# Kernel tuning notes

Measured on AMD Instinct MI355X. Metric: run time of the kernel, lower is better.

## Reference

```python
import jax, jax.numpy as jnp
import numpy as np

# S5 layer: ZOH discretization of diagonal complex SSM + parallel associative scan
# u: (B, L, H) real; state dim P (complex diagonal Lambda)

DT_MIN, DT_MAX = 1e-3, 1e-1
STEP_RESCALE = 1.0

def setup_inputs() -> dict:
    key = jax.random.key(0)
    ks = jax.random.split(key, 7)
    Bsz, L, H, P = 8, 4096, 1024, 512
    u = jax.random.normal(ks[0], (Bsz, L, H), jnp.float32)
    # HiPPO-like diagonal: negative real part, spread imaginary part
    Lambda_re = -0.5 * jnp.abs(jax.random.normal(ks[1], (P,), jnp.float32)) - 0.1
    Lambda_im = jnp.pi * jax.random.normal(ks[2], (P,), jnp.float32)
    # B: (P, H, 2) real/imag stacked (xavier-ish scale); C: (H, P, 2)
    Bp = jax.random.normal(ks[3], (P, H, 2), jnp.float32) / np.sqrt(H)
    Cp = jax.random.normal(ks[4], (H, P, 2), jnp.float32) / np.sqrt(P)
    D = jax.random.normal(ks[5], (H,), jnp.float32)
    log_step = jnp.log(jax.random.uniform(ks[6], (P, 1), jnp.float32) * (DT_MAX - DT_MIN) + DT_MIN)
    return {"u": u, "Lambda_re": Lambda_re, "Lambda_im": Lambda_im,
            "B": Bp, "C": Cp, "D": D, "log_step": log_step}


def _s5_forward(u, Lambda_re, Lambda_im, B, C, D, log_step):
    # clip_eigs=True: keep real part strictly negative
    Lambda = jnp.minimum(Lambda_re, -1e-4) + 1j * Lambda_im          # (P,)
    B_tilde = (B[..., 0] + 1j * B[..., 1]).astype(jnp.complex64)      # (P, H)
    C_tilde = (C[..., 0] + 1j * C[..., 1]).astype(jnp.complex64)      # (H, P)
    step = STEP_RESCALE * jnp.exp(log_step[:, 0])                     # (P,)
    # ZOH discretization
    Lambda_bar = jnp.exp(Lambda * step)                               # (P,)
    B_bar = ((Lambda_bar - 1.0) / Lambda)[:, None] * B_tilde          # (P, H)
    # input projection into state space
    Bu = jnp.einsum('blh,ph->blp', u.astype(jnp.complex64), B_bar)    # (B, L, P)
    A = jnp.broadcast_to(Lambda_bar, Bu.shape)                        # (B, L, P)
    # linear recurrence x_k = Lambda_bar * x_{k-1} + Bu_k via log-depth scan
    def combine(e_i, e_j):
        a_i, b_i = e_i
        a_j, b_j = e_j
        return a_j * a_i, a_j * b_i + b_j
    _, xs = jax.lax.associative_scan(combine, (A, Bu), axis=1)        # (B, L, P)
    # readout
    ys = jnp.einsum('blp,hp->blh', xs, C_tilde).real + D * u          # (B, L, H)
    return ys


def reference(u, Lambda_re, Lambda_im, B, C, D, log_step):
    return _s5_forward(u, Lambda_re, Lambda_im, B, C, D, log_step)
```

## Files before the change

### kernel.cpp

```cpp
#include <hip/hip_runtime.h>


#define Bsz 8
#define Lseq 4096
#define Hdim 1024
#define Pdim 512
#define NCHUNK 64
#define CHUNK 64
#define MROWS 32768

typedef __attribute__((ext_vector_type(8))) __bf16 bf16x8;
typedef __attribute__((ext_vector_type(4))) float f32x4;

__device__ __forceinline__ unsigned short f2bf(float f) {
  union { float f; unsigned u; } v; v.f = f;
  unsigned r = v.u + 0x7fffu + ((v.u >> 16) & 1u);
  return (unsigned short)(r >> 16);
}
__device__ __forceinline__ float bf2f(unsigned short s) {
  union { unsigned u; float f; } v; v.u = ((unsigned)s) << 16;
  return v.f;
}

__device__ __forceinline__ void gld_lds16(const void* g, void* l) {
  __builtin_amdgcn_global_load_lds(
      (const __attribute__((address_space(1))) unsigned int*)g,
      (__attribute__((address_space(3))) unsigned int*)l, 16, 0, 0);
}

__global__ void k_setup(const float* __restrict__ Lre_in, const float* __restrict__ Lim_in,
                        const float* __restrict__ log_step,
                        float2* __restrict__ a_arr, float2* __restrict__ aS_arr,
                        float2* __restrict__ g_arr) {
  int p = threadIdx.x;
  if (p >= Pdim) return;
  float lre = fminf(Lre_in[p], -1e-4f);
  float lim = Lim_in[p];
  float step = expf(log_step[p]);
  float zr = lre * step, zi = lim * step;
  float er = expf(zr);
  float ar = er * cosf(zi), ai = er * sinf(zi);
  a_arr[p] = make_float2(ar, ai);
  float erS = expf(zr * (float)CHUNK);
  aS_arr[p] = make_float2(erS * cosf(zi * (float)CHUNK), erS * sinf(zi * (float)CHUNK));
  float den = lre * lre + lim * lim;
  float nr = ar - 1.0f, ni = ai;
  g_arr[p] = make_float2((nr * lre + ni * lim) / den, (ni * lre - nr * lim) / den);
}

__global__ void k_prep_B(const float* __restrict__ Bin, const float2* __restrict__ g_arr,
                         unsigned short* __restrict__ Bbar2) {
  int idx = blockIdx.x * 256 + threadIdx.x;
  int p = idx >> 10;
  int h = idx & 1023;
  float B0 = Bin[2 * idx];
  float B1 = Bin[2 * idx + 1];
  float2 g = g_arr[p];
  Bbar2[(size_t)p * Hdim + h]            = f2bf(g.x * B0 - g.y * B1);
  Bbar2[(size_t)(Pdim + p) * Hdim + h]   = f2bf(g.x * B1 + g.y * B0);
}

__global__ void k_prep_C(const float* __restrict__ Cin, unsigned short* __restrict__ C2m) {
  int idx = blockIdx.x * 256 + threadIdx.x;
  int h = idx >> 9;
  int p = idx & 511;
  float C0 = Cin[2 * idx];
  float C1 = Cin[2 * idx + 1];
  C2m[(size_t)h * 1024 + p]        = f2bf(C0);
  C2m[(size_t)h * 1024 + 512 + p]  = f2bf(-C1);
}

__global__ void k_cvt_u(const float* __restrict__ u, unsigned short* __restrict__ ub) {
  size_t i = ((size_t)blockIdx.x * 256 + threadIdx.x) * 4;
  float4 v = *(const float4*)(u + i);
  ushort4 o;
  o.x = f2bf(v.x); o.y = f2bf(v.y); o.z = f2bf(v.z); o.w = f2bf(v.w);
  *(ushort4*)(ub + i) = o;
}

template <int EPI>
__global__ __launch_bounds__(256, 5) void gemm_bt(const unsigned short* __restrict__ A,
                                                  const unsigned short* __restrict__ Bt,
                                                  void* __restrict__ Cout,
                                                  const float* __restrict__ uin,
                                                  const float* __restrict__ Dvec) {
  const int K = 1024;
  __shared__ __align__(16) unsigned short sm[16384];
  char* smc = (char*)sm;

  int tid = threadIdx.x;
  int lane = tid & 63;
  int w = tid >> 6;
  int wr = w >> 1, wc = w & 1;
  int quad = lane >> 4;
  int mrow = lane & 15;

  int wg = blockIdx.x;
  size_t rowBase = (size_t)(wg >> 3) * 128;
  size_t colBase = (size_t)(wg & 7) * 128;

  f32x4 acc[4][4];
#pragma unroll
  for (int i = 0; i < 4; i++)
#pragma unroll
    for (int j = 0; j < 4; j++) acc[i][j] = (f32x4){0.f, 0.f, 0.f, 0.f};

  int r0 = tid >> 2;
  int cst = (tid & 3) ^ ((tid >> 3) & 3);
  const unsigned short* pa0 = A + rowBase * K + (size_t)r0 * K + cst * 8;
  const unsigned short* pa1 = pa0 + (size_t)64 * K;
  const unsigned short* pb0 = Bt + colBase * K + (size_t)r0 * K + cst * 8;
  const unsigned short* pb1 = pb0 + (size_t)64 * K;
  int dA0 = w * 1024, dA1 = 4096 + w * 1024;
  int dB0 = 8192 + w * 1024, dB1 = 12288 + w * 1024;

  int cr = quad ^ ((mrow >> 1) & 3);
  int aOff = (wr * 64 + mrow) * 32 + cr * 8;
  int bOff = 4096 + (wc * 64 + mrow) * 32 + cr * 8;

  gld_lds16(pa0, smc + dA0);
  gld_lds16(pa1, smc + dA1);
  gld_lds16(pb0, smc + dB0);
  gld_lds16(pb1, smc + dB1);

  for (int i = 0; i < 32; ++i) {
    __syncthreads();
    int cur = i & 1;
    if (i < 31) {
      int kb = (i + 1) * 32;
      int bb = (cur ^ 1) * 16384;
      gld_lds16(pa0 + kb, smc + bb + dA0);
      gld_lds16(pa1 + kb, smc + bb + dA1);
      gld_lds16(pb0 + kb, smc + bb + dB0);
      gld_lds16(pb1 + kb, smc + bb + dB1);
    }
    const unsigned short* Ab = sm + cur * 8192 + aOff;
    const unsigned short* Bb = sm + cur * 8192 + bOff;
    bf16x8 af[4], bfv[4];
#pragma unroll
    for (int mt = 0; mt < 4; mt++) af[mt] = *(const bf16x8*)(Ab + mt * 512);
#pragma unroll
    for (int nt = 0; nt < 4; nt++) bfv[nt] = *(const bf16x8*)(Bb + nt * 512);
#pragma unroll
    for (int mt = 0; mt < 4; mt++)
#pragma unroll
      for (int nt = 0; nt < 4; nt++)
        acc[mt][nt] = __builtin_amdgcn_mfma_f32_16x16x32_bf16(af[mt], bfv[nt], acc[mt][nt], 0, 0, 0);
  }

  if (EPI == 0) {
    unsigned short* O = (unsigned short*)Cout;
    __syncthreads();
#pragma unroll
    for (int ph = 0; ph < 2; ph++) {
      if (wr == ph) {
#pragma unroll
        for (int mt = 0; mt < 4; mt++)
#pragma unroll
          for (int nt = 0; nt < 4; nt++)
#pragma unroll
            for (int r = 0; r < 4; r++) {
              int lr = mt * 16 + quad * 4 + r;
              int col = wc * 64 + nt * 16 + mrow;
              sm[lr * 136 + col] = f2bf(acc[mt][nt][r]);
            }
      }
      __syncthreads();
#pragma unroll
      for (int it = 0; it < 4; it++) {
        int cid = it * 256 + tid;
        int lr = cid >> 4;
        int cc = cid & 15;
        uint4 v = *(const uint4*)(sm + lr * 136 + cc * 8);
        *(uint4*)(O + (rowBase + ph * 64 + lr) * 1024 + colBase + cc * 8) = v;
      }
      __syncthreads();
    }
  } else {
    float* O = (float*)Cout;
    size_t mBase = rowBase + wr * 64 + quad * 4;
    size_t nBase = colBase + wc * 64 + mrow;
#pragma unroll
    for (int mt = 0; mt < 4; mt++)
#pragma unroll
      for (int nt = 0; nt < 4; nt++) {
        size_t n = nBase + nt * 16;
        float dv = Dvec[n];
#pragma unroll
        for (int r = 0; r < 4; r++) {
          size_t m = mBase + mt * 16 + r;
          O[m * 1024 + n] = acc[mt][nt][r] + dv * uin[m * 1024 + n];
        }
      }
  }
}

__global__ void k_scan1(const unsigned short* __restrict__ Bu, const float2* __restrict__ a_arr,
                        float* __restrict__ carryT) {
  int bc = blockIdx.x;
  int p0 = threadIdx.x * 2;
  int b = bc >> 6, c = bc & 63;
  float2 a0 = a_arr[p0], a1 = a_arr[p0 + 1];
  const unsigned short* bu = Bu + ((size_t)b * Lseq + (size_t)c * CHUNK) * 1024;
  float tr0 = 0.f, ti0 = 0.f, tr1 = 0.f, ti1 = 0.f;
#pragma unroll 8
  for (int l = 0; l < CHUNK; l++) {
    unsigned vr = *(const unsigned*)(bu + (size_t)l * 1024 + p0);
    unsigned vi = *(const unsigned*)(bu + (size_t)l * 1024 + 512 + p0);
    float br0 = bf2f((unsigned short)vr), br1 = bf2f((unsigned short)(vr >> 16));
    float bi0 = bf2f((unsigned short)vi), bi1 = bf2f((unsigned short)(vi >> 16));
    float nr0 = fmaf(a0.x, tr0, fmaf(-a0.y, ti0, br0));
    ti0 = fmaf(a0.x, ti0, fmaf(a0.y, tr0, bi0));
    tr0 = nr0;
    float nr1 = fmaf(a1.x, tr1, fmaf(-a1.y, ti1, br1));
    ti1 = fmaf(a1.x, ti1, fmaf(a1.y, tr1, bi1));
    tr1 = nr1;
  }
  *(float2*)(carryT + (size_t)bc * 1024 + p0) = make_float2(tr0, tr1);
  *(float2*)(carryT + (size_t)bc * 1024 + 512 + p0) = make_float2(ti0, ti1);
}

__global__ void k_scan2(const float* __restrict__ carryT, const float2* __restrict__ aS_arr,
                        float* __restrict__ prefix) {
  int wid = blockIdx.x * 4 + (threadIdx.x >> 6);
  int lane = threadIdx.x & 63;
  int b = wid >> 9;
  int p = wid & 511;
  float2 s = aS_arr[p];
  size_t o = ((size_t)(b * NCHUNK + lane)) * 1024 + p;
  float tr = carryT[o], ti = carryT[o + 512];
  float mr = s.x, mi = s.y;
#pragma unroll
  for (int d = 1; d < 64; d <<= 1) {
    float ur = __shfl_up(tr, d, 64);
    float ui = __shfl_up(ti, d, 64);
    if (lane >= d) {
      tr = fmaf(mr, ur, fmaf(-mi, ui, tr));
      ti = fmaf(mr, ui, fmaf(mi, ur, ti));
    }
    float nmr = mr * mr - mi * mi;
    mi = 2.f * mr * mi;
    mr = nmr;
  }
  float er = __shfl_up(tr, 1, 64);
  float ei = __shfl_up(ti, 1, 64);
  if (lane == 0) { er = 0.f; ei = 0.f; }
  prefix[o] = er;
  prefix[o + 512] = ei;
}

__global__ void k_scan3(const unsigned short* __restrict__ Bu, const float2* __restrict__ a_arr,
                        const float* __restrict__ prefix, unsigned short* __restrict__ xs) {
  int bc = blockIdx.x;
  int p0 = threadIdx.x * 2;
  int b = bc >> 6, c = bc & 63;
  float2 a0 = a_arr[p0], a1 = a_arr[p0 + 1];
  size_t base = ((size_t)b * Lseq + (size_t)c * CHUNK) * 1024;
  size_t po = (size_t)bc * 1024 + p0;
  float2 xrv = *(const float2*)(prefix + po);
  float2 xiv = *(const float2*)(prefix + po + 512);
  float xr0 = xrv.x, xr1 = xrv.y, xi0 = xiv.x, xi1 = xiv.y;
#pragma unroll 8
  for (int l = 0; l < CHUNK; l++) {
    unsigned vr = *(const unsigned*)(Bu + base + (size_t)l * 1024 + p0);
    unsigned vi = *(const unsigned*)(Bu + base + (size_t)l * 1024 + 512 + p0);
    float br0 = bf2f((unsigned short)vr), br1 = bf2f((unsigned short)(vr >> 16));
    float bi0 = bf2f((unsigned short)vi), bi1 = bf2f((unsigned short)(vi >> 16));
    float nr0 = fmaf(a0.x, xr0, fmaf(-a0.y, xi0, br0));
    xi0 = fmaf(a0.x, xi0, fmaf(a0.y, xr0, bi0));
    xr0 = nr0;
    float nr1 = fmaf(a1.x, xr1, fmaf(-a1.y, xi1, br1));
    xi1 = fmaf(a1.x, xi1, fmaf(a1.y, xr1, bi1));
    xr1 = nr1;
    unsigned orv = (unsigned)f2bf(xr0) | ((unsigned)f2bf(xr1) << 16);
    unsigned oiv = (unsigned)f2bf(xi0) | ((unsigned)f2bf(xi1) << 16);
    *(unsigned*)(xs + base + (size_t)l * 1024 + p0) = orv;
    *(unsigned*)(xs + base + (size_t)l * 1024 + 512 + p0) = oiv;
  }
}

extern "C" void kernel_launch(void* const* d_in, const int* in_sizes, int n_in,
                              void* d_out, int out_size, void* d_ws, size_t ws_size,
                              hipStream_t stream) {
  const float* u     = (const float*)d_in[0];
  const float* Lre   = (const float*)d_in[1];
  const float* Lim   = (const float*)d_in[2];
  const float* Bin   = (const float*)d_in[3];
  const float* Cin   = (const float*)d_in[4];
  const float* Dvec  = (const float*)d_in[5];
  const float* lstep = (const float*)d_in[6];

  char* ws = (char*)d_ws;
  unsigned short* ubf_xs = (unsigned short*)(ws);
  unsigned short* Bbar2  = (unsigned short*)(ws + 67108864);
  unsigned short* C2m    = (unsigned short*)(ws + 69206016);
  float*          carryT = (float*)(ws + 71303168);
  float*          prefix = (float*)(ws + 73400320);
  float2*         a_arr  = (float2*)(ws + 75497472);
  float2*         aS_arr = (float2*)(ws + 75501568);
  float2*         g_arr  = (float2*)(ws + 75505664);

  unsigned short* Bu = (unsigned short*)d_out;

  k_setup<<<1, 512, 0, stream>>>(Lre, Lim, lstep, a_arr, aS_arr, g_arr);
  k_prep_B<<<2048, 256, 0, stream>>>(Bin, g_arr, Bbar2);
  k_prep_C<<<2048, 256, 0, stream>>>(Cin, C2m);
  k_cvt_u<<<32768, 256, 0, stream>>>(u, ubf_xs);

  gemm_bt<0><<<2048, 256, 0, stream>>>(ubf_xs, Bbar2, (void*)Bu, nullptr, nullptr);

  k_scan1<<<512, 256, 0, stream>>>(Bu, a_arr, carryT);
  k_scan2<<<1024, 256, 0, stream>>>(carryT, aS_arr, prefix);
  k_scan3<<<512, 256, 0, stream>>>(Bu, a_arr, prefix, ubf_xs);

  gemm_bt<1><<<2048, 256, 0, stream>>>(ubf_xs, C2m, d_out, u, Dvec);
}
```

Measured before the change: 496.8 us.

## Triple-buffer GEMM LDS tiles with two-ahead prefetch and explicit vmcnt waits

```diff
diff --git a/kernel.cpp b/kernel.cpp
--- a/kernel.cpp
+++ b/kernel.cpp
@@ -79,13 +79,13 @@
 }
 
 template <int EPI>
-__global__ __launch_bounds__(256, 5) void gemm_bt(const unsigned short* __restrict__ A,
+__global__ __launch_bounds__(256, 4) void gemm_bt(const unsigned short* __restrict__ A,
                                                   const unsigned short* __restrict__ Bt,
                                                   void* __restrict__ Cout,
                                                   const float* __restrict__ uin,
                                                   const float* __restrict__ Dvec) {
   const int K = 1024;
-  __shared__ __align__(16) unsigned short sm[16384];
+  __shared__ __align__(16) unsigned short sm[24576];
   char* smc = (char*)sm;
 
   int tid = threadIdx.x;
@@ -118,21 +118,27 @@
   int aOff = (wr * 64 + mrow) * 32 + cr * 8;
   int bOff = 4096 + (wc * 64 + mrow) * 32 + cr * 8;
 
-  gld_lds16(pa0, smc + dA0);
-  gld_lds16(pa1, smc + dA1);
-  gld_lds16(pb0, smc + dB0);
-  gld_lds16(pb1, smc + dB1);
-
+#define STAGE_TILE(t, b)                                        \
+  do {                                                          \
+    int kb_ = (t) * 32;                                         \
+    int bb_ = (b) * 16384;                                      \
+    gld_lds16(pa0 + kb_, smc + bb_ + dA0);                      \
+    gld_lds16(pa1 + kb_, smc + bb_ + dA1);                      \
+    gld_lds16(pb0 + kb_, smc + bb_ + dB0);                      \
+    gld_lds16(pb1 + kb_, smc + bb_ + dB1);                      \
+  } while (0)
+
+  STAGE_TILE(0, 0);
+  STAGE_TILE(1, 1);
+
+  int cur = 0;
   for (int i = 0; i < 32; ++i) {
-    __syncthreads();
-    int cur = i & 1;
-    if (i < 31) {
-      int kb = (i + 1) * 32;
-      int bb = (cur ^ 1) * 16384;
-      gld_lds16(pa0 + kb, smc + bb + dA0);
-      gld_lds16(pa1 + kb, smc + bb + dA1);
-      gld_lds16(pb0 + kb, smc + bb + dB0);
-      gld_lds16(pb1 + kb, smc + bb + dB1);
+    if (i < 31) asm volatile("s_waitcnt vmcnt(4)" ::: "memory");
+    else        asm volatile("s_waitcnt vmcnt(0)" ::: "memory");
+    __builtin_amdgcn_s_barrier();
+    if (i < 30) {
+      int nb = cur + 2; if (nb >= 3) nb -= 3;
+      STAGE_TILE(i + 2, nb);
     }
     const unsigned short* Ab = sm + cur * 8192 + aOff;
     const unsigned short* Bb = sm + cur * 8192 + bOff;
@@ -146,7 +152,9 @@
 #pragma unroll
       for (int nt = 0; nt < 4; nt++)
         acc[mt][nt] = __builtin_amdgcn_mfma_f32_16x16x32_bf16(af[mt], bfv[nt], acc[mt][nt], 0, 0, 0);
-  }
+    cur += 1; if (cur == 3) cur = 0;
+  }
+#undef STAGE_TILE
 
   if (EPI == 0) {
     unsigned short* O = (unsigned short*)Cout;
```

After: 502.9 us. No clear change (+1.2%).

## Replace 128x128 GEMM with 256x256 tile, 8-wave, phased pipelined BF16 MFMA kernel

Applied to the files above, without the earlier changes.

```diff
diff --git a/kernel.cpp b/kernel.cpp
--- a/kernel.cpp
+++ b/kernel.cpp
@@ -78,118 +78,151 @@
   *(ushort4*)(ub + i) = o;
 }
 
+
+#define STAGE_A(t_, bo_)                                                    \
+  do {                                                                      \
+    _Pragma("unroll")                                                       \
+    for (int jj = 0; jj < 4; jj++)                                          \
+      gld_lds16(pa[jj] + (t_) * 64, smc + (bo_) + (jj * 512 + tid) * 16);   \
+  } while (0)
+
+#define STAGE_B(t_, bo_)                                                    \
+  do {                                                                      \
+    _Pragma("unroll")                                                       \
+    for (int jj = 0; jj < 4; jj++)                                          \
+      gld_lds16(pb[jj] + (t_) * 64, smc + (bo_) + 32768 + (jj * 512 + tid) * 16); \
+  } while (0)
+
+#define PHASE_Q(mh, nh, PRE, POST)                                          \
+  {                                                                         \
+    const char* bb_ = smc + bufo;                                           \
+    bf16x8 af_[4][2], bf_[2][2];                                            \
+    _Pragma("unroll")                                                       \
+    for (int i_ = 0; i_ < 4; i_++) {                                        \
+      int rb_ = aRowByte + ((mh) * 4 + i_) * 2048;                          \
+      af_[i_][0] = *(const bf16x8*)(bb_ + rb_ + k0);                        \
+      af_[i_][1] = *(const bf16x8*)(bb_ + rb_ + k1);                        \
+    }                                                                       \
+    _Pragma("unroll")                                                       \
+    for (int j_ = 0; j_ < 2; j_++) {                                        \
+      int rb_ = bRowByte + ((nh) * 2 + j_) * 2048;                          \
+      bf_[j_][0] = *(const bf16x8*)(bb_ + rb_ + k0);                        \
+      bf_[j_][1] = *(const bf16x8*)(bb_ + rb_ + k1);                        \
+    }                                                                       \
+    PRE;                                                                    \
+    __builtin_amdgcn_s_barrier();                                           \
+    asm volatile("s_waitcnt lgkmcnt(0)" ::: "memory");                      \
+    __builtin_amdgcn_sched_barrier(0);                                      \
+    __builtin_amdgcn_s_setprio(1);                                          \
+    _Pragma("unroll")                                                       \
+    for (int i_ = 0; i_ < 4; i_++)                                          \
+      _Pragma("unroll")                                                     \
+      for (int j_ = 0; j_ < 2; j_++) {                                      \
+        acc[(mh) * 4 + i_][(nh) * 2 + j_] =                                 \
+            __builtin_amdgcn_mfma_f32_16x16x32_bf16(                        \
+                af_[i_][0], bf_[j_][0], acc[(mh) * 4 + i_][(nh) * 2 + j_], 0, 0, 0); \
+        acc[(mh) * 4 + i_][(nh) * 2 + j_] =                                 \
+            __builtin_amdgcn_mfma_f32_16x16x32_bf16(                        \
+                af_[i_][1], bf_[j_][1], acc[(mh) * 4 + i_][(nh) * 2 + j_], 0, 0, 0); \
+      }                                                                     \
+    __builtin_amdgcn_s_setprio(0);                                          \
+    POST;                                                                   \
+    __builtin_amdgcn_s_barrier();                                           \
+  }
+
 template <int EPI>
-__global__ __launch_bounds__(256, 5) void gemm_bt(const unsigned short* __restrict__ A,
+__global__ __launch_bounds__(512, 2) void gemm256(const unsigned short* __restrict__ A,
                                                   const unsigned short* __restrict__ Bt,
                                                   void* __restrict__ Cout,
                                                   const float* __restrict__ uin,
                                                   const float* __restrict__ Dvec) {
   const int K = 1024;
-  __shared__ __align__(16) unsigned short sm[16384];
+  __shared__ __align__(16) unsigned short sm[65536];
   char* smc = (char*)sm;
 
   int tid = threadIdx.x;
   int lane = tid & 63;
   int w = tid >> 6;
-  int wr = w >> 1, wc = w & 1;
+  int wr = w >> 2, wc = w & 3;
   int quad = lane >> 4;
   int mrow = lane & 15;
 
   int wg = blockIdx.x;
-  size_t rowBase = (size_t)(wg >> 3) * 128;
-  size_t colBase = (size_t)(wg & 7) * 128;
-
-  f32x4 acc[4][4];
-#pragma unroll
-  for (int i = 0; i < 4; i++)
+  size_t rowBase = (size_t)(wg >> 2) * 256;
+  size_t colBase = (size_t)(wg & 3) * 256;
+
+  f32x4 acc[8][4];
+#pragma unroll
+  for (int i = 0; i < 8; i++)
 #pragma unroll
     for (int j = 0; j < 4; j++) acc[i][j] = (f32x4){0.f, 0.f, 0.f, 0.f};
 
-  int r0 = tid >> 2;
-  int cst = (tid & 3) ^ ((tid >> 3) & 3);
-  const unsigned short* pa0 = A + rowBase * K + (size_t)r0 * K + cst * 8;
-  const unsigned short* pa1 = pa0 + (size_t)64 * K;
-  const unsigned short* pb0 = Bt + colBase * K + (size_t)r0 * K + cst * 8;
-  const unsigned short* pb1 = pb0 + (size_t)64 * K;
-  int dA0 = w * 1024, dA1 = 4096 + w * 1024;
-  int dB0 = 8192 + w * 1024, dB1 = 12288 + w * 1024;
-
-  int cr = quad ^ ((mrow >> 1) & 3);
-  int aOff = (wr * 64 + mrow) * 32 + cr * 8;
-  int bOff = 4096 + (wc * 64 + mrow) * 32 + cr * 8;
-
-  gld_lds16(pa0, smc + dA0);
-  gld_lds16(pa1, smc + dA1);
-  gld_lds16(pb0, smc + dB0);
-  gld_lds16(pb1, smc + dB1);
-
-  for (int i = 0; i < 32; ++i) {
-    __syncthreads();
-    int cur = i & 1;
-    if (i < 31) {
-      int kb = (i + 1) * 32;
-      int bb = (cur ^ 1) * 16384;
-      gld_lds16(pa0 + kb, smc + bb + dA0);
-      gld_lds16(pa1 + kb, smc + bb + dA1);
-      gld_lds16(pb0 + kb, smc + bb + dB0);
-      gld_lds16(pb1 + kb, smc + bb + dB1);
-    }
-    const unsigned short* Ab = sm + cur * 8192 + aOff;
-    const unsigned short* Bb = sm + cur * 8192 + bOff;
-    bf16x8 af[4], bfv[4];
-#pragma unroll
-    for (int mt = 0; mt < 4; mt++) af[mt] = *(const bf16x8*)(Ab + mt * 512);
-#pragma unroll
-    for (int nt = 0; nt < 4; nt++) bfv[nt] = *(const bf16x8*)(Bb + nt * 512);
-#pragma unroll
-    for (int mt = 0; mt < 4; mt++)
-#pragma unroll
-      for (int nt = 0; nt < 4; nt++)
-        acc[mt][nt] = __builtin_amdgcn_mfma_f32_16x16x32_bf16(af[mt], bfv[nt], acc[mt][nt], 0, 0, 0);
+  int cs = (tid & 7) ^ ((tid >> 3) & 7);
+  int rT = tid >> 3;
+  const unsigned short* pa[4];
+  const unsigned short* pb[4];
+#pragma unroll
+  for (int jj = 0; jj < 4; jj++) {
+    pa[jj] = A  + (rowBase + jj * 64 + rT) * K + cs * 8;
+    pb[jj] = Bt + (colBase + jj * 64 + rT) * K + cs * 8;
+  }
+
+  int axor = (mrow & 7) << 4;
+  int k0 = (quad * 16) ^ axor;
+  int k1 = (64 + quad * 16) ^ axor;
+  int aRowByte = (wr * 128 + mrow) * 128;
+  int bRowByte = 32768 + (wc * 64 + mrow) * 128;
+
+  STAGE_A(0, 0);
+  STAGE_B(0, 0);
+  asm volatile("s_waitcnt vmcnt(0)" ::: "memory");
+  __builtin_amdgcn_s_barrier();
+
+  for (int t = 0; t < 16; ++t) {
+    int bufo = (t & 1) * 65536;
+    int nbo = bufo ^ 65536;
+    PHASE_Q(0, 0, if (t < 15) STAGE_A(t + 1, nbo), );
+    PHASE_Q(0, 1, if (t < 15) STAGE_B(t + 1, nbo), );
+    PHASE_Q(1, 0, , );
+    PHASE_Q(1, 1, , asm volatile("s_waitcnt vmcnt(0)" ::: "memory"));
   }
 
   if (EPI == 0) {
     unsigned short* O = (unsigned short*)Cout;
     __syncthreads();
 #pragma unroll
-    for (int ph = 0; ph < 2; ph++) {
-      if (wr == ph) {
-#pragma unroll
-        for (int mt = 0; mt < 4; mt++)
-#pragma unroll
-          for (int nt = 0; nt < 4; nt++)
-#pragma unroll
-            for (int r = 0; r < 4; r++) {
-              int lr = mt * 16 + quad * 4 + r;
-              int col = wc * 64 + nt * 16 + mrow;
-              sm[lr * 136 + col] = f2bf(acc[mt][nt][r]);
-            }
-      }
-      __syncthreads();
-#pragma unroll
-      for (int it = 0; it < 4; it++) {
-        int cid = it * 256 + tid;
-        int lr = cid >> 4;
-        int cc = cid & 15;
-        uint4 v = *(const uint4*)(sm + lr * 136 + cc * 8);
-        *(uint4*)(O + (rowBase + ph * 64 + lr) * 1024 + colBase + cc * 8) = v;
-      }
-      __syncthreads();
+    for (int fm = 0; fm < 8; fm++)
+#pragma unroll
+      for (int fn = 0; fn < 4; fn++)
+#pragma unroll
+        for (int r = 0; r < 4; r++) {
+          int m_l = wr * 128 + fm * 16 + quad * 4 + r;
+          int n_l = wc * 64 + fn * 16 + mrow;
+          sm[m_l * 256 + n_l] = f2bf(acc[fm][fn][r]);
+        }
+    __syncthreads();
+#pragma unroll
+    for (int it = 0; it < 16; it++) {
+      int cid = it * 512 + tid;
+      int r = cid >> 5;
+      int c = cid & 31;
+      uint4 v = *(const uint4*)(sm + r * 256 + c * 8);
+      *(uint4*)(O + (rowBase + r) * 1024 + colBase + c * 8) = v;
     }
   } else {
     float* O = (float*)Cout;
-    size_t mBase = rowBase + wr * 64 + quad * 4;
+    size_t mBase = rowBase + wr * 128 + quad * 4;
     size_t nBase = colBase + wc * 64 + mrow;
 #pragma unroll
-    for (int mt = 0; mt < 4; mt++)
-#pragma unroll
-      for (int nt = 0; nt < 4; nt++) {
-        size_t n = nBase + nt * 16;
+    for (int fm = 0; fm < 8; fm++)
+#pragma unroll
+      for (int fn = 0; fn < 4; fn++) {
+        size_t n = nBase + fn * 16;
         float dv = Dvec[n];
 #pragma unroll
         for (int r = 0; r < 4; r++) {
-          size_t m = mBase + mt * 16 + r;
-          O[m * 1024 + n] = acc[mt][nt][r] + dv * uin[m * 1024 + n];
+          size_t m = mBase + fm * 16 + r;
+          O[m * 1024 + n] = acc[fm][fn][r] + dv * uin[m * 1024 + n];
         }
       }
   }
@@ -307,11 +340,11 @@
   k_prep_C<<<2048, 256, 0, stream>>>(Cin, C2m);
   k_cvt_u<<<32768, 256, 0, stream>>>(u, ubf_xs);
 
-  gemm_bt<0><<<2048, 256, 0, stream>>>(ubf_xs, Bbar2, (void*)Bu, nullptr, nullptr);
+  gemm256<0><<<512, 512, 0, stream>>>(ubf_xs, Bbar2, (void*)Bu, nullptr, nullptr);
 
   k_scan1<<<512, 256, 0, stream>>>(Bu, a_arr, carryT);
   k_scan2<<<1024, 256, 0, stream>>>(carryT, aS_arr, prefix);
   k_scan3<<<512, 256, 0, stream>>>(Bu, a_arr, prefix, ubf_xs);
 
-  gemm_bt<1><<<2048, 256, 0, stream>>>(ubf_xs, C2m, d_out, u, Dvec);
-}
+  gemm256<1><<<512, 512, 0, stream>>>(ubf_xs, C2m, d_out, u, Dvec);
+}
```

New measurement: 459.3 us. 7.6% less time.
